# Performance work log

Hardware: AMD Instinct MI355X
Metric: run time of the kernel (lower is better)

## Reference

```python
import jax, jax.numpy as jnp
import numpy as np

N = 65536            # query points (256x256 image)
G = 2048             # number of gaussian/gabor primitives
K = 8                # top-k wave frequencies per primitive
NUM_TOTAL_FREQ = 128
MAX_FREQ = 128.0


def setup_inputs() -> dict:
    key = jax.random.key(0)
    ks = jax.random.split(key, 7)
    x = jax.random.uniform(ks[0], (N, 2), jnp.float32)
    gaussian_colors = 0.05 * jax.random.normal(ks[1], (G, 3), jnp.float32)
    gaussian_positions = jax.random.uniform(ks[2], (G, 2), jnp.float32)
    gaussian_scales = 3.0 + 0.05 * jax.random.normal(ks[3], (G, 2), jnp.float32)
    gaussian_rotations = jnp.pi * jax.random.uniform(ks[4], (G, 1), jnp.float32)
    topk_wave_coefficients = 0.01 * (2.0 * jax.random.uniform(ks[5], (G, K), jnp.float32) - 1.0)
    topk_wave_indices = jax.random.randint(ks[6], (G, K), 0, NUM_TOTAL_FREQ)
    return {
        "x": x,
        "gaussian_colors": gaussian_colors,
        "gaussian_positions": gaussian_positions,
        "gaussian_scales": gaussian_scales,
        "gaussian_rotations": gaussian_rotations,
        "topk_wave_coefficients": topk_wave_coefficients,
        "topk_wave_indices": topk_wave_indices,
    }


def reference(x, gaussian_colors, gaussian_positions, gaussian_scales,
              gaussian_rotations, topk_wave_coefficients, topk_wave_indices):
    # Dense (unblocked) faithful evaluation of the periodic-primitive splat:
    # out[n] = sum_g color_g * exp(-0.5*((rx*sx)^2+(ry*sy)^2)) * sum_k c_gk*cos(2*pi*f_gk*rx)
    dx = x[:, None, 0] - gaussian_positions[None, :, 0]   # [N, G]
    dy = x[:, None, 1] - gaussian_positions[None, :, 1]   # [N, G]
    th = gaussian_rotations[:, 0]                          # [G]
    c, s = jnp.cos(th), jnp.sin(th)
    rx = c[None, :] * dx + s[None, :] * dy                 # rotated coords [N, G]
    ry = -s[None, :] * dx + c[None, :] * dy
    sx = gaussian_scales[None, :, 0]
    sy = gaussian_scales[None, :, 1]
    env = jnp.exp(-0.5 * ((rx * sx) ** 2 + (ry * sy) ** 2))  # gaussian envelope [N, G]
    # frequency of each selected coefficient: idx * max_freq / num_total_freq
    freqs = topk_wave_indices.astype(jnp.float32) * (MAX_FREQ / NUM_TOTAL_FREQ)  # [G, K]
    two_pi = 2.0 * jnp.pi
    wave = jnp.zeros_like(env)
    for k in range(K):  # small fixed loop -> avoids materializing [N, G, K]
        wave = wave + topk_wave_coefficients[:, k][None, :] * jnp.cos(two_pi * freqs[:, k][None, :] * rx)
    return (env * wave) @ gaussian_colors  # [N, 3]
```

## Files before the change

kernel.cpp:

```cpp
#include <hip/hip_runtime.h>
#include <math.h>

#define G_NUM   2048
#define N_PTS   65536
#define K_FREQ  8
#define REC     64
#define CHUNKS  16
#define G_PER_CHUNK (G_NUM / CHUNKS)
#define PACK_BYTES ((size_t)G_NUM * REC * sizeof(float))
#define PART_FLOATS ((size_t)N_PTS * 3)
#define PART_BYTES_OLD (PART_FLOATS * sizeof(float) * CHUNKS)
#define LDS_FLOATS  (G_PER_CHUNK * REC)

#define S_TAB   2048
#define INV_H   (2048.0f / 3.0f)
#define TAB_BLOCKS  (G_NUM * (S_TAB / 256))
#define HIST_BLOCKS 64
#define TAB_BYTES   ((size_t)G_NUM * S_TAB * 16)
#define XS_BYTES    ((size_t)N_PTS * 8)
#define PERM_BYTES  ((size_t)N_PTS * 4)
#define PART4_BYTES ((size_t)CHUNKS * N_PTS * 16)
#define PHIST_BYTES ((size_t)HIST_BLOCKS * 1024 * 4)
#define OFF_TAB   (PACK_BYTES)
#define OFF_XS    (OFF_TAB + TAB_BYTES)
#define OFF_PERM  (OFF_XS + XS_BYTES)
#define OFF_PART4 (OFF_PERM + PERM_BYTES)
#define OFF_PHIST (OFF_PART4 + PART4_BYTES)
#define NEW_TOTAL (OFF_PHIST + PHIST_BYTES)

typedef float v2f __attribute__((ext_vector_type(2)));

#if __has_builtin(__builtin_amdgcn_cosf)
__device__ __forceinline__ float hw_cos_rev(float p) { return __builtin_amdgcn_cosf(p); }
#else
__device__ __forceinline__ float hw_cos_rev(float p) { return __cosf(6.28318530717958648f * p); }
#endif
#if __has_builtin(__builtin_amdgcn_exp2f)
__device__ __forceinline__ float hw_exp2(float p) { return __builtin_amdgcn_exp2f(p); }
#else
__device__ __forceinline__ float hw_exp2(float p) { return exp2f(p); }
#endif
#if __has_builtin(__builtin_amdgcn_fractf)
__device__ __forceinline__ float hw_fract(float p) { return __builtin_amdgcn_fractf(p); }
#else
__device__ __forceinline__ float hw_fract(float p) { return p - floorf(p); }
#endif

__device__ __forceinline__ v2f fma2v(v2f a, v2f b, v2f c) {
#if __has_builtin(__builtin_elementwise_fma)
    return __builtin_elementwise_fma(a, b, c);
#else
    v2f r; r.x = fmaf(a.x, b.x, c.x); r.y = fmaf(a.y, b.y, c.y); return r;
#endif
}

__global__ __launch_bounds__(256) void pack_kernel(
    const float* __restrict__ colors, const float* __restrict__ pos,
    const float* __restrict__ scales, const float* __restrict__ rot,
    const float* __restrict__ coef,   const int* __restrict__ idx,
    float* __restrict__ pack)
{
    int j = blockIdx.x * blockDim.x + threadIdx.x;
    if (j >= G_NUM) return;
    float th = rot[j];
    float c = cosf(th), s = sinf(th);
    float px = pos[2 * j], py = pos[2 * j + 1];
    float sx = scales[2 * j], sy = scales[2 * j + 1];
    const float nhl2e = -0.72134752044448170368f;
    float* r = pack + (size_t)j * REC;
    auto put = [&](int pair, float v) { r[2 * pair] = v; r[2 * pair + 1] = v; };
    put(0, -(c * px + s * py));
    put(1, s * px - c * py);
    put(2, c);
    put(3, s);
    put(4, -s);
    put(5, nhl2e * sx * sx);
    put(6, nhl2e * sy * sy);
    put(7, colors[3 * j]);
    put(8, colors[3 * j + 1]);
    put(9, colors[3 * j + 2]);
#pragma unroll
    for (int k = 0; k < K_FREQ; ++k) {
        put(10 + k, (float)idx[j * K_FREQ + k]);
        put(18 + k, coef[j * K_FREQ + k]);
    }
#pragma unroll
    for (int p = 26; p < 32; ++p) put(p, 0.0f);
}

template <bool USE_PART>
__global__ __launch_bounds__(256, 8) void periodic2d_kernel(
    const float* __restrict__ x, const float* __restrict__ pack,
    float* __restrict__ dst)
{
    __shared__ float lds_rec[LDS_FLOATS];
    {
        const float4* __restrict__ src = (const float4*)
            (pack + (size_t)(blockIdx.y * G_PER_CHUNK) * REC);
        float4* dstl = (float4*)lds_rec;
#pragma unroll
        for (int i = 0; i < LDS_FLOATS / 4 / 256; ++i)
            dstl[threadIdx.x + 256 * i] = src[threadIdx.x + 256 * i];
    }
    __syncthreads();

    const int t = blockIdx.x * 256 + threadIdx.x;
    const int p0 = t;
    const int p1 = t + N_PTS / 4;
    const int p2 = t + N_PTS / 2;
    const int p3 = t + 3 * (N_PTS / 4);
    const float2 q0 = ((const float2*)x)[p0];
    const float2 q1 = ((const float2*)x)[p1];
    const float2 q2 = ((const float2*)x)[p2];
    const float2 q3 = ((const float2*)x)[p3];
    const v2f xiA = {q0.x, q1.x}, yiA = {q0.y, q1.y};
    const v2f xiB = {q2.x, q3.x}, yiB = {q2.y, q3.y};
    v2f a0A = {0.f, 0.f}, a1A = {0.f, 0.f}, a2A = {0.f, 0.f};
    v2f a0B = {0.f, 0.f}, a1B = {0.f, 0.f}, a2B = {0.f, 0.f};

    const v2f* rv = (const v2f*)lds_rec;
#pragma unroll 1
    for (int j = 0; j < G_PER_CHUNK; ++j, rv += REC / 2) {
        const v2f rxA = fma2v(xiA, rv[2], fma2v(yiA, rv[3], rv[0]));
        const v2f rxB = fma2v(xiB, rv[2], fma2v(yiB, rv[3], rv[0]));
        const v2f ryA = fma2v(yiA, rv[2], fma2v(xiA, rv[4], rv[1]));
        const v2f ryB = fma2v(yiB, rv[2], fma2v(xiB, rv[4], rv[1]));
        const v2f eargA = fma2v(ryA * rv[6], ryA, (rxA * rv[5]) * rxA);
        const v2f eargB = fma2v(ryB * rv[6], ryB, (rxB * rv[5]) * rxB);
        v2f envA, envB;
        envA.x = hw_exp2(eargA.x); envA.y = hw_exp2(eargA.y);
        envB.x = hw_exp2(eargB.x); envB.y = hw_exp2(eargB.y);
        v2f waveA = {0.f, 0.f}, waveB = {0.f, 0.f};
#pragma unroll
        for (int k = 0; k < K_FREQ; ++k) {
            const v2f phA = rxA * rv[10 + k];
            const v2f phB = rxB * rv[10 + k];
            v2f cA, cB;
            cA.x = hw_cos_rev(phA.x); cA.y = hw_cos_rev(phA.y);
            cB.x = hw_cos_rev(phB.x); cB.y = hw_cos_rev(phB.y);
            waveA = fma2v(cA, rv[18 + k], waveA);
            waveB = fma2v(cB, rv[18 + k], waveB);
        }
        const v2f wA = envA * waveA;
        const v2f wB = envB * waveB;
        a0A = fma2v(wA, rv[7], a0A);  a0B = fma2v(wB, rv[7], a0B);
        a1A = fma2v(wA, rv[8], a1A);  a1B = fma2v(wB, rv[8], a1B);
        a2A = fma2v(wA, rv[9], a2A);  a2B = fma2v(wB, rv[9], a2B);
    }

    if (USE_PART) {
        float* o = dst + (size_t)blockIdx.y * PART_FLOATS;
        o[3 * p0 + 0] = a0A.x; o[3 * p0 + 1] = a1A.x; o[3 * p0 + 2] = a2A.x;
        o[3 * p1 + 0] = a0A.y; o[3 * p1 + 1] = a1A.y; o[3 * p1 + 2] = a2A.y;
        o[3 * p2 + 0] = a0B.x; o[3 * p2 + 1] = a1B.x; o[3 * p2 + 2] = a2B.x;
        o[3 * p3 + 0] = a0B.y; o[3 * p3 + 1] = a1B.y; o[3 * p3 + 2] = a2B.y;
    } else {
        atomicAdd(&dst[3 * p0 + 0], a0A.x);
        atomicAdd(&dst[3 * p0 + 1], a1A.x);
        atomicAdd(&dst[3 * p0 + 2], a2A.x);
        atomicAdd(&dst[3 * p1 + 0], a0A.y);
        atomicAdd(&dst[3 * p1 + 1], a1A.y);
        atomicAdd(&dst[3 * p1 + 2], a2A.y);
        atomicAdd(&dst[3 * p2 + 0], a0B.x);
        atomicAdd(&dst[3 * p2 + 1], a1B.x);
        atomicAdd(&dst[3 * p2 + 2], a2B.x);
        atomicAdd(&dst[3 * p3 + 0], a0B.y);
        atomicAdd(&dst[3 * p3 + 1], a1B.y);
        atomicAdd(&dst[3 * p3 + 2], a2B.y);
    }
}

__global__ __launch_bounds__(256) void reduce_kernel(
    const float* __restrict__ part, float* __restrict__ out)
{
    const int i = blockIdx.x * 256 + threadIdx.x;
    float4 s = {0.f, 0.f, 0.f, 0.f};
#pragma unroll
    for (int c = 0; c < CHUNKS; ++c) {
        const float4 v = ((const float4*)(part + (size_t)c * PART_FLOATS))[i];
        s.x += v.x; s.y += v.y; s.z += v.z; s.w += v.w;
    }
    ((float4*)out)[i] = s;
}


__device__ __forceinline__ int cell_id(float px, float py) {
    int cx = (int)(px * 32.f); cx = cx > 31 ? 31 : cx;
    int cy = (int)(py * 32.f); cy = cy > 31 ? 31 : cy;
    int m = 0;
#pragma unroll
    for (int b = 0; b < 5; ++b)
        m |= (((cx >> b) & 1) << (2 * b)) | (((cy >> b) & 1) << (2 * b + 1));
    return m;
}

__global__ __launch_bounds__(256) void build_hist_kernel(
    const float* __restrict__ colors, const float* __restrict__ pos,
    const float* __restrict__ scales, const float* __restrict__ rot,
    const float* __restrict__ coef,   const int* __restrict__ idx,
    const float* __restrict__ x,
    float* __restrict__ pack, float* __restrict__ tab,
    int* __restrict__ phist)
{
    __shared__ int h[1024];
    const int b = blockIdx.x;
    if (b >= TAB_BLOCKS) {
        const int r = b - TAB_BLOCKS;
#pragma unroll
        for (int i = 0; i < 4; ++i) h[threadIdx.x + 256 * i] = 0;
        __syncthreads();
        const float4* xv = (const float4*)x + (size_t)r * 512;
#pragma unroll
        for (int it = 0; it < 2; ++it) {
            const float4 p = xv[threadIdx.x + 256 * it];
            atomicAdd(&h[cell_id(p.x, p.y)], 1);
            atomicAdd(&h[cell_id(p.z, p.w)], 1);
        }
        __syncthreads();
        int* row = phist + r * 1024;
#pragma unroll
        for (int i = 0; i < 4; ++i)
            row[threadIdx.x + 256 * i] = h[threadIdx.x + 256 * i];
        return;
    }
    const int g  = b >> 3;
    const int bx = b & 7;
    if (bx == 0 && threadIdx.x == 0) {
        float th = rot[g];
        float c = cosf(th), s = sinf(th);
        float px = pos[2 * g], py = pos[2 * g + 1];
        float sx = scales[2 * g], sy = scales[2 * g + 1];
        const float nhl2e = -0.72134752044448170368f;
        float* r = pack + (size_t)g * REC;
        auto put = [&](int pair, float v) { r[2 * pair] = v; r[2 * pair + 1] = v; };
        put(0, -(c * px + s * py));
        put(1, s * px - c * py);
        put(2, c); put(3, s); put(4, -s);
        put(5, nhl2e * sx * sx);
        put(6, nhl2e * sy * sy);
        put(7, colors[3 * g]); put(8, colors[3 * g + 1]); put(9, colors[3 * g + 2]);
    }
    const int i = bx * 256 + threadIdx.x;
    float nk[K_FREQ], ck[K_FREQ];
#pragma unroll
    for (int k = 0; k < K_FREQ; ++k) {
        nk[k] = (float)idx[g * K_FREQ + k];
        ck[k] = coef[g * K_FREQ + k];
    }
    float w[4];
#pragma unroll
    for (int m = 0; m < 4; ++m) {
        const float xm = (float)(3 * i + m - 3072) * 0x1p-11f;
        float acc = 0.f;
#pragma unroll
        for (int k = 0; k < K_FREQ; ++k)
            acc = fmaf(ck[k], hw_cos_rev(nk[k] * xm), acc);
        w[m] = acc;
    }
    const float d1 = w[1] - w[0];
    const float d2 = w[2] - 2.f * w[1] + w[0];
    const float d3 = w[3] - 3.f * w[2] + 3.f * w[1] - w[0];
    float4 o;
    o.x = w[0];
    o.y = 3.f * d1 - 1.5f * d2 + d3;
    o.z = 4.5f * (d2 - d3);
    o.w = 4.5f * d3;
    ((float4*)tab)[(size_t)g * S_TAB + i] = o;
}

__global__ __launch_bounds__(256) void scatter_kernel(
    const float* __restrict__ x, const int* __restrict__ phist,
    float* __restrict__ xs, int* __restrict__ perm)
{
    __shared__ int e[256];
    __shared__ int cur[1024];
    const int r = blockIdx.x;
    const int t = threadIdx.x;
    int4 tot = {0, 0, 0, 0}, base = {0, 0, 0, 0};
#pragma unroll 1
    for (int rr = 0; rr < HIST_BLOCKS; ++rr) {
        const int4 v = ((const int4*)(phist + rr * 1024))[t];
        if (rr < r) { base.x += v.x; base.y += v.y; base.z += v.z; base.w += v.w; }
        tot.x += v.x; tot.y += v.y; tot.z += v.z; tot.w += v.w;
    }
    const int s4 = tot.x + tot.y + tot.z + tot.w;
    e[t] = s4;
    __syncthreads();
#pragma unroll 1
    for (int d = 1; d < 256; d <<= 1) {
        const int a = (t >= d) ? e[t - d] : 0;
        __syncthreads();
        e[t] += a;
        __syncthreads();
    }
    const int excl = e[t] - s4;
    cur[4 * t + 0] = excl + base.x;
    cur[4 * t + 1] = excl + tot.x + base.y;
    cur[4 * t + 2] = excl + tot.x + tot.y + base.z;
    cur[4 * t + 3] = excl + tot.x + tot.y + tot.z + base.w;
    __syncthreads();
    const float4* xv = (const float4*)x + (size_t)r * 512;
#pragma unroll
    for (int it = 0; it < 2; ++it) {
        const int li = t + 256 * it;
        const float4 p = xv[li];
        const int i0 = 2 * (r * 512 + li);
        int pos = atomicAdd(&cur[cell_id(p.x, p.y)], 1);
        ((float2*)xs)[pos] = make_float2(p.x, p.y);
        perm[pos] = i0;
        pos = atomicAdd(&cur[cell_id(p.z, p.w)], 1);
        ((float2*)xs)[pos] = make_float2(p.z, p.w);
        perm[pos] = i0 + 1;
    }
}

struct PipeSet {
    v2f envA, envB, tfA, tfB;
    float4 cA0, cA1, cB0, cB1;
    v2f col0, col1, col2;
};

__global__ __launch_bounds__(256, 4) void periodic2d_tab_kernel(
    const float* __restrict__ xs, const float* __restrict__ pack,
    const float* __restrict__ tab, float* __restrict__ part)
{
    __shared__ float lds_rec[G_PER_CHUNK * 32];
    {
        const float4* __restrict__ src = (const float4*)
            (pack + (size_t)(blockIdx.y * G_PER_CHUNK) * REC);
        float4* d4 = (float4*)lds_rec;
#pragma unroll
        for (int it = 0; it < G_PER_CHUNK * 32 / 4 / 256; ++it) {
            const int i = threadIdx.x + 256 * it;
            d4[i] = src[((i >> 3) << 4) | (i & 7)];
        }
    }
    __syncthreads();

    const int t = blockIdx.x * 256 + threadIdx.x;
    const int p0 = ((t >> 6) << 8) | (t & 63);
    const float2 q0 = ((const float2*)xs)[p0];
    const float2 q1 = ((const float2*)xs)[p0 + 64];
    const float2 q2 = ((const float2*)xs)[p0 + 128];
    const float2 q3 = ((const float2*)xs)[p0 + 192];
    const v2f xiA = {q0.x, q1.x}, yiA = {q0.y, q1.y};
    const v2f xiB = {q2.x, q3.x}, yiB = {q2.y, q3.y};
    v2f a0A = {0.f, 0.f}, a1A = {0.f, 0.f}, a2A = {0.f, 0.f};
    v2f a0B = {0.f, 0.f}, a1B = {0.f, 0.f}, a2B = {0.f, 0.f};
    const v2f vinvh = {INV_H, INV_H};
    const v2f voff  = {1024.f, 1024.f};

    const v2f* __restrict__ rv = (const v2f*)lds_rec;
    const float4* __restrict__ tb =
        (const float4*)tab + (size_t)(blockIdx.y * G_PER_CHUNK) * S_TAB;

    PipeSet s0, s1;

    auto ISSUE = [&](PipeSet& S, const v2f* __restrict__ r,
                     const float4* __restrict__ tbl) {
        const v2f rxA = fma2v(xiA, r[2], fma2v(yiA, r[3], r[0]));
        const v2f rxB = fma2v(xiB, r[2], fma2v(yiB, r[3], r[0]));
        const v2f ryA = fma2v(yiA, r[2], fma2v(xiA, r[4], r[1]));
        const v2f ryB = fma2v(yiB, r[2], fma2v(xiB, r[4], r[1]));
        const v2f eargA = fma2v(ryA * r[6], ryA, (rxA * r[5]) * rxA);
        const v2f eargB = fma2v(ryB * r[6], ryB, (rxB * r[5]) * rxB);
        S.envA.x = hw_exp2(eargA.x); S.envA.y = hw_exp2(eargA.y);
        S.envB.x = hw_exp2(eargB.x); S.envB.y = hw_exp2(eargB.y);
        const v2f uA = fma2v(rxA, vinvh, voff);
        const v2f uB = fma2v(rxB, vinvh, voff);
        const int iA0 = (int)uA.x, iA1 = (int)uA.y;
        const int iB0 = (int)uB.x, iB1 = (int)uB.y;
        S.tfA.x = hw_fract(uA.x); S.tfA.y = hw_fract(uA.y);
        S.tfB.x = hw_fract(uB.x); S.tfB.y = hw_fract(uB.y);
        S.cA0 = tbl[iA0]; S.cA1 = tbl[iA1];
        S.cB0 = tbl[iB0]; S.cB1 = tbl[iB1];
        S.col0 = r[7]; S.col1 = r[8]; S.col2 = r[9];
    };

    auto CONSUME = [&](PipeSet& S) {
        v2f wvA, wvB;
        wvA.x = fmaf(fmaf(fmaf(S.cA0.w, S.tfA.x, S.cA0.z), S.tfA.x, S.cA0.y), S.tfA.x, S.cA0.x);
        wvA.y = fmaf(fmaf(fmaf(S.cA1.w, S.tfA.y, S.cA1.z), S.tfA.y, S.cA1.y), S.tfA.y, S.cA1.x);
        wvB.x = fmaf(fmaf(fmaf(S.cB0.w, S.tfB.x, S.cB0.z), S.tfB.x, S.cB0.y), S.tfB.x, S.cB0.x);
        wvB.y = fmaf(fmaf(fmaf(S.cB1.w, S.tfB.y, S.cB1.z), S.tfB.y, S.cB1.y), S.tfB.y, S.cB1.x);
        const v2f wA = S.envA * wvA;
        const v2f wB = S.envB * wvB;
        a0A = fma2v(wA, S.col0, a0A);  a0B = fma2v(wB, S.col0, a0B);
        a1A = fma2v(wA, S.col1, a1A);  a1B = fma2v(wB, S.col1, a1B);
        a2A = fma2v(wA, S.col2, a2A);  a2B = fma2v(wB, S.col2, a2B);
    };

    ISSUE(s0, rv,      tb);
    ISSUE(s1, rv + 16, tb + S_TAB);
#pragma unroll 1
    for (int j = 0; j < G_PER_CHUNK - 2; j += 2) {
        CONSUME(s0);
        ISSUE(s0, rv + 16 * (j + 2), tb + (size_t)S_TAB * (j + 2));
        CONSUME(s1);
        ISSUE(s1, rv + 16 * (j + 3), tb + (size_t)S_TAB * (j + 3));
    }
    CONSUME(s0);
    CONSUME(s1);

    float4* o = (float4*)part + (size_t)blockIdx.y * N_PTS;
    o[p0      ] = make_float4(a0A.x, a1A.x, a2A.x, 0.f);
    o[p0 +  64] = make_float4(a0A.y, a1A.y, a2A.y, 0.f);
    o[p0 + 128] = make_float4(a0B.x, a1B.x, a2B.x, 0.f);
    o[p0 + 192] = make_float4(a0B.y, a1B.y, a2B.y, 0.f);
}

__global__ __launch_bounds__(256) void reduce_tab_kernel(
    const float* __restrict__ part, const int* __restrict__ perm,
    float* __restrict__ out)
{
    const int p = blockIdx.x * 256 + threadIdx.x;
    const float4* p4 = (const float4*)part;
    float sx = 0.f, sy = 0.f, sz = 0.f;
#pragma unroll
    for (int c = 0; c < CHUNKS; ++c) {
        const float4 v = p4[(size_t)c * N_PTS + p];
        sx += v.x; sy += v.y; sz += v.z;
    }
    const int q = perm[p];
    out[3 * q    ] = sx;
    out[3 * q + 1] = sy;
    out[3 * q + 2] = sz;
}

extern "C" void kernel_launch(void* const* d_in, const int* in_sizes, int n_in,
                              void* d_out, int out_size, void* d_ws, size_t ws_size,
                              hipStream_t stream)
{
    const float* x      = (const float*)d_in[0];
    const float* colors = (const float*)d_in[1];
    const float* pos    = (const float*)d_in[2];
    const float* scales = (const float*)d_in[3];
    const float* rot    = (const float*)d_in[4];
    const float* coef   = (const float*)d_in[5];
    const int*   idx    = (const int*)d_in[6];
    float* out  = (float*)d_out;
    float* pack = (float*)d_ws;

    if (ws_size >= NEW_TOTAL) {
        float* tab   = (float*)((char*)d_ws + OFF_TAB);
        float* xs    = (float*)((char*)d_ws + OFF_XS);
        int*   perm  = (int*)  ((char*)d_ws + OFF_PERM);
        float* part  = (float*)((char*)d_ws + OFF_PART4);
        int*   phist = (int*)  ((char*)d_ws + OFF_PHIST);
        build_hist_kernel<<<dim3(TAB_BLOCKS + HIST_BLOCKS), 256, 0, stream>>>(
            colors, pos, scales, rot, coef, idx, x, pack, tab, phist);
        scatter_kernel<<<dim3(HIST_BLOCKS), 256, 0, stream>>>(x, phist, xs, perm);
        periodic2d_tab_kernel<<<dim3(N_PTS / 1024, CHUNKS), 256, 0, stream>>>(
            xs, pack, tab, part);
        reduce_tab_kernel<<<dim3(N_PTS / 256), 256, 0, stream>>>(part, perm, out);
        return;
    }

    float* part = (float*)((char*)d_ws + PACK_BYTES);
    pack_kernel<<<dim3((G_NUM + 255) / 256), 256, 0, stream>>>(
        colors, pos, scales, rot, coef, idx, pack);
    if (ws_size >= PACK_BYTES + PART_BYTES_OLD) {
        periodic2d_kernel<true><<<dim3(N_PTS / 1024, CHUNKS), 256, 0, stream>>>(
            x, pack, part);
        reduce_kernel<<<dim3((N_PTS * 3 / 4) / 256), 256, 0, stream>>>(part, out);
    } else {
        (void)hipMemsetAsync(d_out, 0, (size_t)out_size * sizeof(float), stream);
        periodic2d_kernel<false><<<dim3(N_PTS / 1024, CHUNKS), 256, 0, stream>>>(
            x, pack, out);
    }
}
```

Measured before the change: 191.7 us.

## Fuse reduction into main kernel via last-block counter; coarsen table build blocks

The separate reduce kernel is removed. Each periodic2d block now fences, bumps a per-column done counter, and the last of the CHUNKS blocks sums all partials and scatters the result to out. The done counters are reset by the scatter kernel. The table build now uses one block per primitive that loops over 8 segments instead of 8 blocks per primitive, and the histogram prefix loop is unrolled. This saves one kernel launch and some redundant per-block setup, at the cost of a serialized tail reduction done by only 64 blocks and extra fences.

```diff
diff --git a/kernel.cpp b/kernel.cpp
--- a/kernel.cpp
+++ b/kernel.cpp
@@ -14,19 +14,20 @@
 
 #define S_TAB   2048
 #define INV_H   (2048.0f / 3.0f)
-#define TAB_BLOCKS  (G_NUM * (S_TAB / 256))
 #define HIST_BLOCKS 64
 #define TAB_BYTES   ((size_t)G_NUM * S_TAB * 16)
 #define XS_BYTES    ((size_t)N_PTS * 8)
 #define PERM_BYTES  ((size_t)N_PTS * 4)
 #define PART4_BYTES ((size_t)CHUNKS * N_PTS * 16)
 #define PHIST_BYTES ((size_t)HIST_BLOCKS * 1024 * 4)
+#define DONE_BYTES  ((size_t)HIST_BLOCKS * 4)
 #define OFF_TAB   (PACK_BYTES)
 #define OFF_XS    (OFF_TAB + TAB_BYTES)
 #define OFF_PERM  (OFF_XS + XS_BYTES)
 #define OFF_PART4 (OFF_PERM + PERM_BYTES)
 #define OFF_PHIST (OFF_PART4 + PART4_BYTES)
-#define NEW_TOTAL (OFF_PHIST + PHIST_BYTES)
+#define OFF_DONE  (OFF_PHIST + PHIST_BYTES)
+#define NEW_TOTAL (OFF_DONE + DONE_BYTES)
 
 typedef float v2f __attribute__((ext_vector_type(2)));
 
@@ -204,8 +205,8 @@
 {
     __shared__ int h[1024];
     const int b = blockIdx.x;
-    if (b >= TAB_BLOCKS) {
-        const int r = b - TAB_BLOCKS;
+    if (b >= G_NUM) {
+        const int r = b - G_NUM;
 #pragma unroll
         for (int i = 0; i < 4; ++i) h[threadIdx.x + 256 * i] = 0;
         __syncthreads();
@@ -223,9 +224,8 @@
             row[threadIdx.x + 256 * i] = h[threadIdx.x + 256 * i];
         return;
     }
-    const int g  = b >> 3;
-    const int bx = b & 7;
-    if (bx == 0 && threadIdx.x == 0) {
+    const int g = b;
+    if (threadIdx.x == 0) {
         float th = rot[g];
         float c = cosf(th), s = sinf(th);
         float px = pos[2 * g], py = pos[2 * g + 1];
@@ -240,44 +240,49 @@
         put(6, nhl2e * sy * sy);
         put(7, colors[3 * g]); put(8, colors[3 * g + 1]); put(9, colors[3 * g + 2]);
     }
-    const int i = bx * 256 + threadIdx.x;
     float nk[K_FREQ], ck[K_FREQ];
 #pragma unroll
     for (int k = 0; k < K_FREQ; ++k) {
         nk[k] = (float)idx[g * K_FREQ + k];
         ck[k] = coef[g * K_FREQ + k];
     }
-    float w[4];
-#pragma unroll
-    for (int m = 0; m < 4; ++m) {
-        const float xm = (float)(3 * i + m - 3072) * 0x1p-11f;
-        float acc = 0.f;
-#pragma unroll
-        for (int k = 0; k < K_FREQ; ++k)
-            acc = fmaf(ck[k], hw_cos_rev(nk[k] * xm), acc);
-        w[m] = acc;
-    }
-    const float d1 = w[1] - w[0];
-    const float d2 = w[2] - 2.f * w[1] + w[0];
-    const float d3 = w[3] - 3.f * w[2] + 3.f * w[1] - w[0];
-    float4 o;
-    o.x = w[0];
-    o.y = 3.f * d1 - 1.5f * d2 + d3;
-    o.z = 4.5f * (d2 - d3);
-    o.w = 4.5f * d3;
-    ((float4*)tab)[(size_t)g * S_TAB + i] = o;
+    float4* tg = (float4*)tab + (size_t)g * S_TAB;
+#pragma unroll 1
+    for (int kk = 0; kk < S_TAB / 256; ++kk) {
+        const int i = threadIdx.x + 256 * kk;
+        float w[4];
+#pragma unroll
+        for (int m = 0; m < 4; ++m) {
+            const float xm = (float)(3 * i + m - 3072) * 0x1p-11f;
+            float acc = 0.f;
+#pragma unroll
+            for (int k = 0; k < K_FREQ; ++k)
+                acc = fmaf(ck[k], hw_cos_rev(nk[k] * xm), acc);
+            w[m] = acc;
+        }
+        const float d1 = w[1] - w[0];
+        const float d2 = w[2] - 2.f * w[1] + w[0];
+        const float d3 = w[3] - 3.f * w[2] + 3.f * w[1] - w[0];
+        float4 o;
+        o.x = w[0];
+        o.y = 3.f * d1 - 1.5f * d2 + d3;
+        o.z = 4.5f * (d2 - d3);
+        o.w = 4.5f * d3;
+        tg[i] = o;
+    }
 }
 
 __global__ __launch_bounds__(256) void scatter_kernel(
     const float* __restrict__ x, const int* __restrict__ phist,
-    float* __restrict__ xs, int* __restrict__ perm)
+    float* __restrict__ xs, int* __restrict__ perm, int* __restrict__ done)
 {
     __shared__ int e[256];
     __shared__ int cur[1024];
     const int r = blockIdx.x;
     const int t = threadIdx.x;
+    if (t == 0) done[r] = 0;
     int4 tot = {0, 0, 0, 0}, base = {0, 0, 0, 0};
-#pragma unroll 1
+#pragma unroll 8
     for (int rr = 0; rr < HIST_BLOCKS; ++rr) {
         const int4 v = ((const int4*)(phist + rr * 1024))[t];
         if (rr < r) { base.x += v.x; base.y += v.y; base.z += v.z; base.w += v.w; }
@@ -322,7 +327,9 @@
 
 __global__ __launch_bounds__(256, 4) void periodic2d_tab_kernel(
     const float* __restrict__ xs, const float* __restrict__ pack,
-    const float* __restrict__ tab, float* __restrict__ part)
+    const float* __restrict__ tab, float* __restrict__ part,
+    const int* __restrict__ perm, float* __restrict__ out,
+    int* __restrict__ done)
 {
     __shared__ float lds_rec[G_PER_CHUNK * 32];
     {
@@ -407,24 +414,31 @@
     o[p0 +  64] = make_float4(a0A.y, a1A.y, a2A.y, 0.f);
     o[p0 + 128] = make_float4(a0B.x, a1B.x, a2B.x, 0.f);
     o[p0 + 192] = make_float4(a0B.y, a1B.y, a2B.y, 0.f);
-}
-
-__global__ __launch_bounds__(256) void reduce_tab_kernel(
-    const float* __restrict__ part, const int* __restrict__ perm,
-    float* __restrict__ out)
-{
-    const int p = blockIdx.x * 256 + threadIdx.x;
-    const float4* p4 = (const float4*)part;
-    float sx = 0.f, sy = 0.f, sz = 0.f;
-#pragma unroll
-    for (int c = 0; c < CHUNKS; ++c) {
-        const float4 v = p4[(size_t)c * N_PTS + p];
-        sx += v.x; sy += v.y; sz += v.z;
-    }
-    const int q = perm[p];
-    out[3 * q    ] = sx;
-    out[3 * q + 1] = sy;
-    out[3 * q + 2] = sz;
+
+    __threadfence();
+    __shared__ int amLast;
+    if (threadIdx.x == 0)
+        amLast = (atomicAdd(&done[blockIdx.x], 1) == CHUNKS - 1);
+    __syncthreads();
+    if (amLast) {
+        __threadfence();
+        const float4* pp = (const float4*)part;
+        const int pbase = blockIdx.x * 1024 + threadIdx.x;
+#pragma unroll 1
+        for (int k = 0; k < 4; ++k) {
+            const int p = pbase + 256 * k;
+            float sx = 0.f, sy = 0.f, sz = 0.f;
+#pragma unroll
+            for (int c = 0; c < CHUNKS; ++c) {
+                const float4 v = pp[(size_t)c * N_PTS + p];
+                sx += v.x; sy += v.y; sz += v.z;
+            }
+            const int q = perm[p];
+            out[3 * q    ] = sx;
+            out[3 * q + 1] = sy;
+            out[3 * q + 2] = sz;
+        }
+    }
 }
 
 extern "C" void kernel_launch(void* const* d_in, const int* in_sizes, int n_in,
@@ -447,12 +461,13 @@
         int*   perm  = (int*)  ((char*)d_ws + OFF_PERM);
         float* part  = (float*)((char*)d_ws + OFF_PART4);
         int*   phist = (int*)  ((char*)d_ws + OFF_PHIST);
-        build_hist_kernel<<<dim3(TAB_BLOCKS + HIST_BLOCKS), 256, 0, stream>>>(
+        int*   done  = (int*)  ((char*)d_ws + OFF_DONE);
+        build_hist_kernel<<<dim3(G_NUM + HIST_BLOCKS), 256, 0, stream>>>(
             colors, pos, scales, rot, coef, idx, x, pack, tab, phist);
-        scatter_kernel<<<dim3(HIST_BLOCKS), 256, 0, stream>>>(x, phist, xs, perm);
+        scatter_kernel<<<dim3(HIST_BLOCKS), 256, 0, stream>>>(
+            x, phist, xs, perm, done);
         periodic2d_tab_kernel<<<dim3(N_PTS / 1024, CHUNKS), 256, 0, stream>>>(
-            xs, pack, tab, part);
-        reduce_tab_kernel<<<dim3(N_PTS / 256), 256, 0, stream>>>(part, perm, out);
+            xs, pack, tab, part, perm, out, done);
         return;
     }
 
```

Result: slower. 302.8 us (+57.9%).
